# Performance work log

Hardware: AMD Instinct MI355X
Metric: run time of the kernel (lower is better)

## Reference

```python
import jax, jax.numpy as jnp
import numpy as np

EPS = 1e-8        # slot-attention epsilon
LN_EPS = 1e-5     # torch LayerNorm default
NUM_ITERS = 3

def _ln(x, g, b):
    m = jnp.mean(x, axis=-1, keepdims=True)
    v = jnp.var(x, axis=-1, keepdims=True)
    return (x - m) * jax.lax.rsqrt(v + LN_EPS) * g + b

def setup_inputs() -> dict:
    key = jax.random.key(0)
    ks = jax.random.split(key, 24)
    B, N, D, S, K, H = 64, 4096, 256, 256, 8, 512
    sc = 0.02
    return {
        "inputs": jax.random.normal(ks[0], (B, N, D), dtype=jnp.float32),
        "noise": jax.random.normal(ks[1], (B, K, S), dtype=jnp.float32),
        "slot_mu": jax.random.normal(ks[2], (1, 1, S)) * sc,
        "slot_log_sigma": jax.random.normal(ks[3], (1, 1, S)) * sc,
        "g_in": jnp.ones((D,)), "b_in": jnp.zeros((D,)),
        "g_sl": jnp.ones((S,)), "b_sl": jnp.zeros((S,)),
        "g_mlp": jnp.ones((S,)), "b_mlp": jnp.zeros((S,)),
        "Wq": jax.random.normal(ks[4], (S, S)) * sc,
        "Wk": jax.random.normal(ks[5], (S, D)) * sc,
        "Wv": jax.random.normal(ks[6], (S, D)) * sc,
        "W_ih": jax.random.normal(ks[7], (3 * S, S)) * sc,
        "W_hh": jax.random.normal(ks[8], (3 * S, S)) * sc,
        "b_ih": jnp.zeros((3 * S,)), "b_hh": jnp.zeros((3 * S,)),
        "W1": jax.random.normal(ks[9], (H, S)) * sc,
        "b1": jnp.zeros((H,)),
        "W2": jax.random.normal(ks[10], (S, H)) * sc,
        "b2": jnp.zeros((S,)),
    }

def _gru_cell(x, h, W_ih, W_hh, b_ih, b_hh):
    gi = x @ W_ih.T + b_ih
    gh = h @ W_hh.T + b_hh
    ir, iz, inn = jnp.split(gi, 3, axis=-1)
    hr, hz, hn = jnp.split(gh, 3, axis=-1)
    r = jax.nn.sigmoid(ir + hr)
    z = jax.nn.sigmoid(iz + hz)
    n = jnp.tanh(inn + r * hn)
    return (1.0 - z) * n + z * h

def reference(inputs, noise, slot_mu, slot_log_sigma, g_in, b_in, g_sl, b_sl,
              g_mlp, b_mlp, Wq, Wk, Wv, W_ih, W_hh, b_ih, b_hh, W1, b1, W2, b2):
    S = Wq.shape[0]
    slots = slot_mu + jnp.exp(slot_log_sigma) * noise          # [B,K,S]
    x = _ln(inputs, g_in, b_in)                                # [B,N,D]
    k = (x @ Wk.T) * (S ** -0.5)                               # [B,N,S]
    v = x @ Wv.T                                               # [B,N,S]
    for i in range(NUM_ITERS):
        slots_prev = slots
        q = _ln(slots, g_sl, b_sl) @ Wq.T                      # [B,K,S]
        attn_logits = jnp.einsum('bns,bks->bnk', k, q)         # [B,N,K]
        attn = jax.nn.softmax(attn_logits, axis=-1) + EPS      # softmax over slots
        attn = attn / jnp.sum(attn, axis=1, keepdims=True)     # normalize over inputs
        updates = jnp.einsum('bnk,bns->bks', attn, v)          # [B,K,S]
        slots = _gru_cell(updates, slots_prev, W_ih, W_hh, b_ih, b_hh)
        if i < NUM_ITERS - 1:
            h = jax.nn.relu(_ln(slots, g_mlp, b_mlp) @ W1.T + b1)
            slots = slots + (h @ W2.T + b2)
    return slots
```

## Files before the change

kernel.cpp:

```cpp
#include <hip/hip_runtime.h>
#include <math.h>

#define NB 64
#define NN 4096
#define ND 256
#define NS 256
#define NK 8
#define NH 512
#define NROW (NB*NN)
#define NSLOT (NB*NK)
#define EPSA 1e-8f
#define NCG 64

typedef unsigned short u16;
typedef unsigned int   u32;
typedef __bf16 bf16x8 __attribute__((ext_vector_type(8)));
typedef float  f32x4  __attribute__((ext_vector_type(4)));

__device__ __forceinline__ float bf2f(u16 u) {
  union { u32 i; float f; } v; v.i = ((u32)u) << 16; return v.f;
}
__device__ __forceinline__ u16 f2bf(float f) {
  union { float f; u32 i; } v; v.f = f;
  u32 x = v.i;
  return (u16)((x + 0x7FFFu + ((x >> 16) & 1u)) >> 16);
}
__device__ __forceinline__ u32 pack2(float a, float b) {
  return (u32)f2bf(a) | ((u32)f2bf(b) << 16);
}

#define OFF_XBF    0ULL
#define OFF_KG     134217728ULL
#define OFF_VTG    268435456ULL
#define OFF_SLOTS  402653184ULL
#define OFF_QBF    403177472ULL
#define OFF_UPDP   403439616ULL
#define OFF_SUMSP  436994048ULL
#define OFF_WC     437125120ULL
#define OFF_WQT    437387264ULL
#define OFF_WIHT   437649408ULL
#define OFF_WHHT   438435840ULL
#define OFF_W1T    439222272ULL
#define OFF_W2T    439746560ULL

__global__ __launch_bounds__(256) void prep_kernel(
    const float* __restrict__ Wq, const float* __restrict__ Wk, const float* __restrict__ Wv,
    const float* __restrict__ Wih, const float* __restrict__ Whh,
    const float* __restrict__ W1, const float* __restrict__ W2,
    u16* __restrict__ Wc, float* __restrict__ WqT, float* __restrict__ WihT,
    float* __restrict__ WhhT, float* __restrict__ W1T, float* __restrict__ W2T)
{
  int idx = blockIdx.x * 256 + threadIdx.x;
  if (idx < 512*256) {
    int j = idx >> 8, d = idx & 255;
    float w = (j < 256) ? Wk[idx] * 0.0625f : Wv[idx - 65536];
    Wc[idx] = f2bf(w);
    W1T[d*512 + j] = W1[idx];
  }
  if (idx < 256*256) {
    int j = idx >> 8, d = idx & 255;
    WqT[d*256 + j] = Wq[idx];
  }
  if (idx < 768*256) {
    int j = idx >> 8, d = idx & 255;
    WihT[d*768 + j] = Wih[idx];
    WhhT[d*768 + j] = Whh[idx];
  }
  if (idx < 256*512) {
    int j = idx >> 9, h = idx & 511;
    W2T[h*256 + j] = W2[idx];
  }
}

__global__ __launch_bounds__(256) void slots_init_kernel(
    const float* __restrict__ noise, const float* __restrict__ mu,
    const float* __restrict__ lsig, float* __restrict__ slots)
{
  int idx = blockIdx.x * 256 + threadIdx.x;
  int s = idx & 255;
  slots[idx] = mu[s] + expf(lsig[s]) * noise[idx];
}

__global__ __launch_bounds__(256) void ln_cast_kernel(
    const float* __restrict__ x, const float* __restrict__ g, const float* __restrict__ bb,
    u16* __restrict__ out)
{
  int row = blockIdx.x * 4 + (threadIdx.x >> 6);
  int lane = threadIdx.x & 63;
  float4 xv = *(const float4*)(x + (size_t)row * 256 + lane * 4);
  float s  = xv.x + xv.y + xv.z + xv.w;
  float sq = xv.x*xv.x + xv.y*xv.y + xv.z*xv.z + xv.w*xv.w;
  #pragma unroll
  for (int m = 32; m >= 1; m >>= 1) { s += __shfl_xor(s, m, 64); sq += __shfl_xor(sq, m, 64); }
  float mean = s * (1.f/256.f);
  float rstd = rsqrtf(sq * (1.f/256.f) - mean*mean + 1e-5f);
  float4 gv = *(const float4*)(g + lane*4);
  float4 bv = *(const float4*)(bb + lane*4);
  ushort4 o;
  o.x = f2bf((xv.x - mean) * rstd * gv.x + bv.x);
  o.y = f2bf((xv.y - mean) * rstd * gv.y + bv.y);
  o.z = f2bf((xv.z - mean) * rstd * gv.z + bv.z);
  o.w = f2bf((xv.w - mean) * rstd * gv.w + bv.w);
  *(ushort4*)(out + (size_t)row * 256 + lane*4) = o;
}

__global__ __launch_bounds__(256) void gemm_kv_kernel(
    const u16* __restrict__ A, const u16* __restrict__ Bt,
    u16* __restrict__ kg, u16* __restrict__ vtg)
{
  __shared__ u16 smem[17408];
  u16* As = smem;
  u16* Bs = smem + 4096;
  const int tid = threadIdx.x;
  const int lane = tid & 63;
  const int wv = tid >> 6;
  const int bm = blockIdx.x;
  const int bn = blockIdx.y;
  const int wm = (wv & 1) * 64;
  const int wn = (wv >> 1) * 64;

  f32x4 acc[4][4] = {};

  for (int k0 = 0; k0 < 256; k0 += 32) {
    #pragma unroll
    for (int r = 0; r < 2; ++r) {
      int off = ((r*4 + wv) << 10) + lane*16;
      int row = off >> 6;
      int col = (off & 63) >> 1;
      const u16* ga = A  + (size_t)(bm*128 + row) * 256 + k0 + col;
      const u16* gb = Bt + (size_t)(bn*128 + row) * 256 + k0 + col;
      __builtin_amdgcn_global_load_lds(
        (const __attribute__((address_space(1))) u32*)ga,
        (__attribute__((address_space(3))) u32*)((char*)As + off), 16, 0, 0);
      __builtin_amdgcn_global_load_lds(
        (const __attribute__((address_space(1))) u32*)gb,
        (__attribute__((address_space(3))) u32*)((char*)Bs + off), 16, 0, 0);
    }
    __syncthreads();
    bf16x8 af[4], bfr[4];
    #pragma unroll
    for (int t4 = 0; t4 < 4; ++t4) {
      af[t4]  = *(const bf16x8*)&As[(wm + t4*16 + (lane & 15)) * 32 + (lane >> 4) * 8];
      bfr[t4] = *(const bf16x8*)&Bs[(wn + t4*16 + (lane & 15)) * 32 + (lane >> 4) * 8];
    }
    #pragma unroll
    for (int mt = 0; mt < 4; ++mt)
      #pragma unroll
      for (int nt = 0; nt < 4; ++nt)
        acc[mt][nt] = __builtin_amdgcn_mfma_f32_16x16x32_bf16(af[mt], bfr[nt], acc[mt][nt], 0, 0, 0);
    __syncthreads();
  }
  const int cr = (lane >> 4) * 4;
  const int cc = lane & 15;
  if (bn < 2) {
    #pragma unroll
    for (int mt = 0; mt < 4; ++mt)
      #pragma unroll
      for (int nt = 0; nt < 4; ++nt)
        #pragma unroll
        for (int r = 0; r < 4; ++r) {
          size_t row = (size_t)(bm*128 + wm + mt*16 + cr + r);
          int col = bn*128 + wn + nt*16 + cc;
          kg[row * 256 + col] = f2bf(acc[mt][nt][r]);
        }
  } else {
    #pragma unroll
    for (int mt = 0; mt < 4; ++mt)
      #pragma unroll
      for (int nt = 0; nt < 4; ++nt) {
        int c  = wn + nt*16 + cc;
        int r0 = wm + mt*16 + cr;
        u32* p = (u32*)&smem[c*136 + r0];
        p[0] = pack2(acc[mt][nt][0], acc[mt][nt][1]);
        p[1] = pack2(acc[mt][nt][2], acc[mt][nt][3]);
      }
    __syncthreads();
    int c = tid >> 1, half = tid & 1;
    int d = (bn - 2) * 128 + c;
    const u16* srcp = &smem[c*136 + half*64];
    u16* dstp = vtg + (size_t)(bm >> 5)*1048576 + (size_t)d*4096 + (bm & 31)*128 + half*64;
    #pragma unroll
    for (int i = 0; i < 8; ++i)
      *(uint4*)(dstp + i*8) = *(const uint4*)(srcp + i*8);
  }
}

__global__ __launch_bounds__(256) void q_kernel(
    const float* __restrict__ slots, const float* __restrict__ gw, const float* __restrict__ bw,
    const float* __restrict__ WqT, u16* __restrict__ qbf)
{
  __shared__ float ln[2][256];
  int t = threadIdx.x, wv = t >> 6, lane = t & 63;
  int base = blockIdx.x * 2;
  if (wv < 2) {
    int row = base + wv;
    float4 xv = *(const float4*)(slots + (size_t)row*256 + lane*4);
    float s  = xv.x + xv.y + xv.z + xv.w;
    float sq = xv.x*xv.x + xv.y*xv.y + xv.z*xv.z + xv.w*xv.w;
    #pragma unroll
    for (int m = 32; m >= 1; m >>= 1) { s += __shfl_xor(s, m, 64); sq += __shfl_xor(sq, m, 64); }
    float mean = s * (1.f/256.f);
    float rstd = rsqrtf(sq * (1.f/256.f) - mean*mean + 1e-5f);
    float4 gv = *(const float4*)(gw + lane*4);
    float4 bv = *(const float4*)(bw + lane*4);
    ln[wv][lane*4+0] = (xv.x - mean)*rstd*gv.x + bv.x;
    ln[wv][lane*4+1] = (xv.y - mean)*rstd*gv.y + bv.y;
    ln[wv][lane*4+2] = (xv.z - mean)*rstd*gv.z + bv.z;
    ln[wv][lane*4+3] = (xv.w - mean)*rstd*gv.w + bv.w;
  }
  __syncthreads();
  float a0 = 0.f, a1 = 0.f;
  for (int d = 0; d < 256; ++d) {
    float w = WqT[d*256 + t];
    a0 += ln[0][d] * w;
    a1 += ln[1][d] * w;
  }
  qbf[(size_t)base*256 + t]     = f2bf(a0);
  qbf[(size_t)(base+1)*256 + t] = f2bf(a1);
}

__global__ __launch_bounds__(256) void attn_kernel(
    const u16* __restrict__ kg, const u16* __restrict__ vtg, const u16* __restrict__ qbf,
    float* __restrict__ updp, float* __restrict__ sums_p)
{
  __shared__ u16 tile[16384];
  __shared__ u16 attnT[16*72];
  __shared__ float sums_w[4][8];
  const int b = blockIdx.x, cg = blockIdx.y;
  const int t = threadIdx.x, w = t >> 6, lane = t & 63;
  const int L15 = lane & 15, q4 = lane >> 4;
  const int n0 = cg*64;
  const int slot = L15 & 7;

  bf16x8 vb[2][4];
  #pragma unroll
  for (int ks = 0; ks < 2; ++ks)
    #pragma unroll
    for (int dt = 0; dt < 4; ++dt) {
      int d = (dt*4 + w)*16 + L15;
      vb[ks][dt] = *(const bf16x8*)(vtg + (size_t)b*1048576 + (size_t)d*4096 + n0 + ks*32 + q4*8);
    }
  bf16x8 qf[8];
  {
    const u16* qp = qbf + ((size_t)b*8 + slot)*256;
    #pragma unroll
    for (int ks = 0; ks < 8; ++ks)
      qf[ks] = *(const bf16x8*)(qp + ks*32 + q4*8);
  }
  {
    const u16* srcbase = kg + (size_t)(b*4096 + n0)*256;
    #pragma unroll
    for (int j = 0; j < 8; ++j) {
      int i = w*8 + j;
      int n = i*2 + (lane >> 5);
      int p = lane & 31;
      int c = (p & 24) | ((p ^ n) & 7);
      const u16* src = srcbase + (size_t)n*256 + c*8;
      __builtin_amdgcn_global_load_lds(
        (const __attribute__((address_space(1))) u32*)src,
        (__attribute__((address_space(3))) u32*)((char*)tile + i*1024 + lane*16), 16, 0, 0);
    }
  }
  __syncthreads();

  f32x4 lg = {};
  {
    int n = w*16 + L15;
    #pragma unroll
    for (int ks = 0; ks < 8; ++ks) {
      int cck = ks*4 + q4;
      int p = (cck & 24) | ((cck ^ n) & 7);
      bf16x8 af = *(const bf16x8*)&tile[n*256 + p*8];
      lg = __builtin_amdgcn_mfma_f32_16x16x32_bf16(af, qf[ks], lg, 0, 0, 0);
    }
  }
  float av[4], tot = 0.f;
  #pragma unroll
  for (int r = 0; r < 4; ++r) {
    float val = lg[r];
    float mx = val;
    mx = fmaxf(mx, __shfl_xor(mx, 1, 64));
    mx = fmaxf(mx, __shfl_xor(mx, 2, 64));
    mx = fmaxf(mx, __shfl_xor(mx, 4, 64));
    float e = expf(val - mx);
    float se = e;
    se += __shfl_xor(se, 1, 64);
    se += __shfl_xor(se, 2, 64);
    se += __shfl_xor(se, 4, 64);
    av[r] = e / se + EPSA;
    tot += av[r];
  }
  if (L15 < 8) {
    u32* p = (u32*)&attnT[L15*72 + w*16 + q4*4];
    p[0] = pack2(av[0], av[1]);
    p[1] = pack2(av[2], av[3]);
  }
  tot += __shfl_xor(tot, 16, 64);
  tot += __shfl_xor(tot, 32, 64);
  if (q4 == 0 && L15 < 8) sums_w[w][L15] = tot;
  __syncthreads();

  f32x4 accp[4] = {};
  #pragma unroll
  for (int ks = 0; ks < 2; ++ks) {
    bf16x8 pa = *(const bf16x8*)&attnT[slot*72 + ks*32 + q4*8];
    #pragma unroll
    for (int dt = 0; dt < 4; ++dt)
      accp[dt] = __builtin_amdgcn_mfma_f32_16x16x32_bf16(pa, vb[ks][dt], accp[dt], 0, 0, 0);
  }
  if (q4 < 2) {
    float* up = updp + ((size_t)(b*NCG + cg))*2048;
    #pragma unroll
    for (int dt = 0; dt < 4; ++dt) {
      int d = (dt*4 + w)*16 + L15;
      #pragma unroll
      for (int r = 0; r < 4; ++r)
        up[(q4*4 + r)*256 + d] = accp[dt][r];
    }
  }
  if (t < 8)
    sums_p[(b*NCG + cg)*8 + t] = sums_w[0][t] + sums_w[1][t] + sums_w[2][t] + sums_w[3][t];
}

__global__ __launch_bounds__(256) void grumlp_kernel(
    const float* __restrict__ updp, const float* __restrict__ sums_p,
    const float* __restrict__ WihT, const float* __restrict__ WhhT,
    const float* __restrict__ bih, const float* __restrict__ bhh,
    const float* __restrict__ gm, const float* __restrict__ bm,
    const float* __restrict__ W1T, const float* __restrict__ b1,
    const float* __restrict__ W2T, const float* __restrict__ b2,
    float* __restrict__ slots, int do_mlp)
{
  __shared__ float xs[4][256], hs[4][256];
  __shared__ float ln[4][256];
  __shared__ float hb[4][512];
  int t = threadIdx.x, w = t >> 6, lane = t & 63;
  int base = blockIdx.x * 4;
  #pragma unroll
  for (int g = 0; g < 4; ++g) {
    int row = base + g;
    int b = row >> 3, s = row & 7;
    float u = 0.f, sm = 0.f;
    for (int c = 0; c < NCG; ++c) {
      u  += updp[((size_t)(b*NCG + c)*8 + s)*256 + t];
      sm += sums_p[(b*NCG + c)*8 + s];
    }
    xs[g][t] = u / sm;
    hs[g][t] = slots[(size_t)row*256 + t];
  }
  __syncthreads();
  float ra[4] = {}, za[4] = {}, ia[4] = {}, ha[4] = {};
  for (int d = 0; d < 256; ++d) {
    float wir = WihT[d*768 + t], wiz = WihT[d*768 + 256 + t], win = WihT[d*768 + 512 + t];
    float whr = WhhT[d*768 + t], whz = WhhT[d*768 + 256 + t], whn = WhhT[d*768 + 512 + t];
    #pragma unroll
    for (int g = 0; g < 4; ++g) {
      float xx = xs[g][d], hh = hs[g][d];
      ra[g] += xx*wir + hh*whr;
      za[g] += xx*wiz + hh*whz;
      ia[g] += xx*win;
      ha[g] += hh*whn;
    }
  }
  float bir = bih[t], biz = bih[256+t], bin = bih[512+t];
  float bhr = bhh[t], bhz = bhh[256+t], bhn = bhh[512+t];
  float nv[4];
  #pragma unroll
  for (int g = 0; g < 4; ++g) {
    float r  = 1.f/(1.f + expf(-(ra[g] + bir + bhr)));
    float z  = 1.f/(1.f + expf(-(za[g] + biz + bhz)));
    float nn = tanhf(ia[g] + bin + r*(ha[g] + bhn));
    nv[g] = (1.f - z)*nn + z*hs[g][t];
  }
  if (!do_mlp) {
    #pragma unroll
    for (int g = 0; g < 4; ++g)
      slots[(size_t)(base+g)*256 + t] = nv[g];
    return;
  }
  #pragma unroll
  for (int g = 0; g < 4; ++g) xs[g][t] = nv[g];
  __syncthreads();
  {
    float4 xv = *(const float4*)&xs[w][lane*4];
    float s  = xv.x + xv.y + xv.z + xv.w;
    float sq = xv.x*xv.x + xv.y*xv.y + xv.z*xv.z + xv.w*xv.w;
    #pragma unroll
    for (int m = 32; m >= 1; m >>= 1) { s += __shfl_xor(s, m, 64); sq += __shfl_xor(sq, m, 64); }
    float mean = s * (1.f/256.f);
    float rstd = rsqrtf(sq * (1.f/256.f) - mean*mean + 1e-5f);
    float4 gv = *(const float4*)(gm + lane*4);
    float4 bv = *(const float4*)(bm + lane*4);
    ln[w][lane*4+0] = (xv.x - mean)*rstd*gv.x + bv.x;
    ln[w][lane*4+1] = (xv.y - mean)*rstd*gv.y + bv.y;
    ln[w][lane*4+2] = (xv.z - mean)*rstd*gv.z + bv.z;
    ln[w][lane*4+3] = (xv.w - mean)*rstd*gv.w + bv.w;
  }
  __syncthreads();
  float h0[4] = {}, h1[4] = {};
  for (int d = 0; d < 256; ++d) {
    float w0 = W1T[d*512 + t], w1 = W1T[d*512 + 256 + t];
    #pragma unroll
    for (int g = 0; g < 4; ++g) { float l = ln[g][d]; h0[g] += l*w0; h1[g] += l*w1; }
  }
  float bb0 = b1[t], bb1 = b1[256 + t];
  #pragma unroll
  for (int g = 0; g < 4; ++g) {
    hb[g][t]       = fmaxf(h0[g] + bb0, 0.f);
    hb[g][256 + t] = fmaxf(h1[g] + bb1, 0.f);
  }
  __syncthreads();
  float o[4] = {};
  for (int hh = 0; hh < 512; ++hh) {
    float ww = W2T[hh*256 + t];
    #pragma unroll
    for (int g = 0; g < 4; ++g) o[g] += hb[g][hh] * ww;
  }
  float b2v = b2[t];
  #pragma unroll
  for (int g = 0; g < 4; ++g)
    slots[(size_t)(base+g)*256 + t] = xs[g][t] + o[g] + b2v;
}

extern "C" void kernel_launch(void* const* d_in, const int* in_sizes, int n_in,
                              void* d_out, int out_size, void* d_ws, size_t ws_size,
                              hipStream_t stream)
{
  (void)in_sizes; (void)n_in; (void)out_size; (void)ws_size;
  const float* inputs = (const float*)d_in[0];
  const float* noise  = (const float*)d_in[1];
  const float* mu     = (const float*)d_in[2];
  const float* lsig   = (const float*)d_in[3];
  const float* g_in   = (const float*)d_in[4];
  const float* b_in   = (const float*)d_in[5];
  const float* g_sl   = (const float*)d_in[6];
  const float* b_sl   = (const float*)d_in[7];
  const float* g_mlp  = (const float*)d_in[8];
  const float* b_mlp  = (const float*)d_in[9];
  const float* Wq     = (const float*)d_in[10];
  const float* Wk     = (const float*)d_in[11];
  const float* Wv     = (const float*)d_in[12];
  const float* Wih    = (const float*)d_in[13];
  const float* Whh    = (const float*)d_in[14];
  const float* bih    = (const float*)d_in[15];
  const float* bhh    = (const float*)d_in[16];
  const float* W1     = (const float*)d_in[17];
  const float* b1     = (const float*)d_in[18];
  const float* W2     = (const float*)d_in[19];
  const float* b2     = (const float*)d_in[20];

  char* ws = (char*)d_ws;
  u16*   x_bf   = (u16*)  (ws + OFF_XBF);
  u16*   kg     = (u16*)  (ws + OFF_KG);
  u16*   vtg    = (u16*)  (ws + OFF_VTG);
  float* slots  = (float*)(ws + OFF_SLOTS);
  u16*   qb     = (u16*)  (ws + OFF_QBF);
  float* updp   = (float*)(ws + OFF_UPDP);
  float* sums_p = (float*)(ws + OFF_SUMSP);
  u16*   Wc     = (u16*)  (ws + OFF_WC);
  float* WqT    = (float*)(ws + OFF_WQT);
  float* WihT   = (float*)(ws + OFF_WIHT);
  float* WhhT   = (float*)(ws + OFF_WHHT);
  float* W1T    = (float*)(ws + OFF_W1T);
  float* W2T    = (float*)(ws + OFF_W2T);

  prep_kernel<<<768, 256, 0, stream>>>(Wq, Wk, Wv, Wih, Whh, W1, W2,
                                       Wc, WqT, WihT, WhhT, W1T, W2T);
  slots_init_kernel<<<512, 256, 0, stream>>>(noise, mu, lsig, slots);
  ln_cast_kernel<<<NROW/4, 256, 0, stream>>>(inputs, g_in, b_in, x_bf);
  gemm_kv_kernel<<<dim3(NROW/128, 4), 256, 0, stream>>>(x_bf, Wc, kg, vtg);

  for (int it = 0; it < 3; ++it) {
    q_kernel<<<NSLOT/2, 256, 0, stream>>>(slots, g_sl, b_sl, WqT, qb);
    attn_kernel<<<dim3(NB, NCG), 256, 0, stream>>>(kg, vtg, qb, updp, sums_p);
    grumlp_kernel<<<NSLOT/4, 256, 0, stream>>>(updp, sums_p, WihT, WhhT, bih, bhh,
                                               g_mlp, b_mlp, W1T, b1, W2T, b2,
                                               slots, (it < 2) ? 1 : 0);
  }
  hipMemcpyAsync(d_out, slots, (size_t)NSLOT*NS*sizeof(float),
                 hipMemcpyDeviceToDevice, stream);
}
```

Before: 1.131 ms.

## Store K/V in MFMA-fragment layout, enlarge attention chunks, fuse q-projection into GRU kernel

The KV GEMM now writes K and V directly in a pre-tiled layout that matches the MFMA fragment order. Each attention block can then load operand fragments straight from global memory without staging through LDS. Attention blocks now cover 256 inputs instead of 64, which cuts the partial-sum count the GRU kernel must reduce, and the GEMM grid is flattened. The slot LayerNorm and Wq projection move into the tail of the GRU/MLP kernel, removing a launch per iteration. In exchange, the GRU kernel handles 2 slots per block, doubling its block count and weight re-reads, and the scattered 2-byte stores in the GEMM epilogue may be less efficient.

```diff
diff --git a/kernel.cpp b/kernel.cpp
--- a/kernel.cpp
+++ b/kernel.cpp
@@ -10,16 +10,13 @@
 #define NROW (NB*NN)
 #define NSLOT (NB*NK)
 #define EPSA 1e-8f
-#define NCG 64
+#define NCG 16
 
 typedef unsigned short u16;
 typedef unsigned int   u32;
 typedef __bf16 bf16x8 __attribute__((ext_vector_type(8)));
 typedef float  f32x4  __attribute__((ext_vector_type(4)));
 
-__device__ __forceinline__ float bf2f(u16 u) {
-  union { u32 i; float f; } v; v.i = ((u32)u) << 16; return v.f;
-}
 __device__ __forceinline__ u16 f2bf(float f) {
   union { float f; u32 i; } v; v.f = f;
   u32 x = v.i;
@@ -30,18 +27,18 @@
 }
 
 #define OFF_XBF    0ULL
-#define OFF_KG     134217728ULL
-#define OFF_VTG    268435456ULL
+#define OFF_KPRE   134217728ULL
+#define OFF_VPRE   268435456ULL
 #define OFF_SLOTS  402653184ULL
 #define OFF_QBF    403177472ULL
 #define OFF_UPDP   403439616ULL
-#define OFF_SUMSP  436994048ULL
-#define OFF_WC     437125120ULL
-#define OFF_WQT    437387264ULL
-#define OFF_WIHT   437649408ULL
-#define OFF_WHHT   438435840ULL
-#define OFF_W1T    439222272ULL
-#define OFF_W2T    439746560ULL
+#define OFF_SUMSP  411828224ULL
+#define OFF_WC     411860992ULL
+#define OFF_WQT    412123136ULL
+#define OFF_WIHT   412385280ULL
+#define OFF_WHHT   413171712ULL
+#define OFF_W1T    413958144ULL
+#define OFF_W2T    414482432ULL
 
 __global__ __launch_bounds__(256) void prep_kernel(
     const float* __restrict__ Wq, const float* __restrict__ Wk, const float* __restrict__ Wv,
@@ -106,16 +103,15 @@
 
 __global__ __launch_bounds__(256) void gemm_kv_kernel(
     const u16* __restrict__ A, const u16* __restrict__ Bt,
-    u16* __restrict__ kg, u16* __restrict__ vtg)
-{
-  __shared__ u16 smem[17408];
-  u16* As = smem;
-  u16* Bs = smem + 4096;
+    u16* __restrict__ kpre, u16* __restrict__ vpre)
+{
+  __shared__ u16 As[4096];
+  __shared__ u16 Bs[4096];
   const int tid = threadIdx.x;
   const int lane = tid & 63;
   const int wv = tid >> 6;
-  const int bm = blockIdx.x;
-  const int bn = blockIdx.y;
+  const int bm = blockIdx.x >> 2;
+  const int bn = blockIdx.x & 3;
   const int wm = (wv & 1) * 64;
   const int wn = (wv >> 1) * 64;
 
@@ -154,34 +150,34 @@
   const int cc = lane & 15;
   if (bn < 2) {
     #pragma unroll
-    for (int mt = 0; mt < 4; ++mt)
+    for (int mt = 0; mt < 4; ++mt) {
+      int ntile = bm*8 + (wm >> 4) + mt;
       #pragma unroll
-      for (int nt = 0; nt < 4; ++nt)
+      for (int nt = 0; nt < 4; ++nt) {
+        int d = bn*128 + wn + nt*16 + cc;
+        size_t base = ((size_t)ntile*8 + (d >> 5))*512 + ((d >> 3) & 3)*8 + (d & 7);
+        #pragma unroll
+        for (int r = 0; r < 4; ++r)
+          kpre[base + (cr + r)*32] = f2bf(acc[mt][nt][r]);
+      }
+    }
+  } else {
+    #pragma unroll
+    for (int mt = 0; mt < 4; ++mt) {
+      #pragma unroll
+      for (int nt = 0; nt < 4; ++nt) {
+        int dv = (bn - 2)*128 + wn + nt*16 + cc;
         #pragma unroll
         for (int r = 0; r < 4; ++r) {
-          size_t row = (size_t)(bm*128 + wm + mt*16 + cr + r);
-          int col = bn*128 + wn + nt*16 + cc;
-          kg[row * 256 + col] = f2bf(acc[mt][nt][r]);
+          int n = bm*128 + wm + mt*16 + cr + r;
+          int b = n >> 12, nn = n & 4095;
+          size_t addr = (size_t)b*1048576
+                      + ((size_t)(dv >> 4)*128 + (nn >> 5))*512
+                      + (dv & 15)*32 + ((nn >> 3) & 3)*8 + (nn & 7);
+          vpre[addr] = f2bf(acc[mt][nt][r]);
         }
-  } else {
-    #pragma unroll
-    for (int mt = 0; mt < 4; ++mt)
-      #pragma unroll
-      for (int nt = 0; nt < 4; ++nt) {
-        int c  = wn + nt*16 + cc;
-        int r0 = wm + mt*16 + cr;
-        u32* p = (u32*)&smem[c*136 + r0];
-        p[0] = pack2(acc[mt][nt][0], acc[mt][nt][1]);
-        p[1] = pack2(acc[mt][nt][2], acc[mt][nt][3]);
       }
-    __syncthreads();
-    int c = tid >> 1, half = tid & 1;
-    int d = (bn - 2) * 128 + c;
-    const u16* srcp = &smem[c*136 + half*64];
-    u16* dstp = vtg + (size_t)(bm >> 5)*1048576 + (size_t)d*4096 + (bm & 31)*128 + half*64;
-    #pragma unroll
-    for (int i = 0; i < 8; ++i)
-      *(uint4*)(dstp + i*8) = *(const uint4*)(srcp + i*8);
+    }
   }
 }
 
@@ -220,26 +216,16 @@
 }
 
 __global__ __launch_bounds__(256) void attn_kernel(
-    const u16* __restrict__ kg, const u16* __restrict__ vtg, const u16* __restrict__ qbf,
+    const u16* __restrict__ kpre, const u16* __restrict__ vpre, const u16* __restrict__ qbf,
     float* __restrict__ updp, float* __restrict__ sums_p)
 {
-  __shared__ u16 tile[16384];
-  __shared__ u16 attnT[16*72];
+  __shared__ u16 attnT[8*264];
   __shared__ float sums_w[4][8];
   const int b = blockIdx.x, cg = blockIdx.y;
   const int t = threadIdx.x, w = t >> 6, lane = t & 63;
   const int L15 = lane & 15, q4 = lane >> 4;
-  const int n0 = cg*64;
   const int slot = L15 & 7;
 
-  bf16x8 vb[2][4];
-  #pragma unroll
-  for (int ks = 0; ks < 2; ++ks)
-    #pragma unroll
-    for (int dt = 0; dt < 4; ++dt) {
-      int d = (dt*4 + w)*16 + L15;
-      vb[ks][dt] = *(const bf16x8*)(vtg + (size_t)b*1048576 + (size_t)d*4096 + n0 + ks*32 + q4*8);
-    }
   bf16x8 qf[8];
   {
     const u16* qp = qbf + ((size_t)b*8 + slot)*256;
@@ -247,53 +233,39 @@
     for (int ks = 0; ks < 8; ++ks)
       qf[ks] = *(const bf16x8*)(qp + ks*32 + q4*8);
   }
-  {
-    const u16* srcbase = kg + (size_t)(b*4096 + n0)*256;
-    #pragma unroll
-    for (int j = 0; j < 8; ++j) {
-      int i = w*8 + j;
-      int n = i*2 + (lane >> 5);
-      int p = lane & 31;
-      int c = (p & 24) | ((p ^ n) & 7);
-      const u16* src = srcbase + (size_t)n*256 + c*8;
-      __builtin_amdgcn_global_load_lds(
-        (const __attribute__((address_space(1))) u32*)src,
-        (__attribute__((address_space(3))) u32*)((char*)tile + i*1024 + lane*16), 16, 0, 0);
-    }
-  }
-  __syncthreads();
-
-  f32x4 lg = {};
-  {
-    int n = w*16 + L15;
+
+  const u16* kbase = kpre + (size_t)(b*256 + cg*16)*8*512 + L15*32 + q4*8;
+  float tot = 0.f;
+  #pragma unroll
+  for (int i = 0; i < 4; ++i) {
+    f32x4 lg = {};
+    const u16* ktile = kbase + (size_t)(w*4 + i)*8*512;
     #pragma unroll
     for (int ks = 0; ks < 8; ++ks) {
-      int cck = ks*4 + q4;
-      int p = (cck & 24) | ((cck ^ n) & 7);
-      bf16x8 af = *(const bf16x8*)&tile[n*256 + p*8];
+      bf16x8 af = *(const bf16x8*)(ktile + ks*512);
       lg = __builtin_amdgcn_mfma_f32_16x16x32_bf16(af, qf[ks], lg, 0, 0, 0);
     }
-  }
-  float av[4], tot = 0.f;
-  #pragma unroll
-  for (int r = 0; r < 4; ++r) {
-    float val = lg[r];
-    float mx = val;
-    mx = fmaxf(mx, __shfl_xor(mx, 1, 64));
-    mx = fmaxf(mx, __shfl_xor(mx, 2, 64));
-    mx = fmaxf(mx, __shfl_xor(mx, 4, 64));
-    float e = expf(val - mx);
-    float se = e;
-    se += __shfl_xor(se, 1, 64);
-    se += __shfl_xor(se, 2, 64);
-    se += __shfl_xor(se, 4, 64);
-    av[r] = e / se + EPSA;
-    tot += av[r];
-  }
-  if (L15 < 8) {
-    u32* p = (u32*)&attnT[L15*72 + w*16 + q4*4];
-    p[0] = pack2(av[0], av[1]);
-    p[1] = pack2(av[2], av[3]);
+    float av[4];
+    #pragma unroll
+    for (int r = 0; r < 4; ++r) {
+      float val = lg[r];
+      float mx = val;
+      mx = fmaxf(mx, __shfl_xor(mx, 1, 64));
+      mx = fmaxf(mx, __shfl_xor(mx, 2, 64));
+      mx = fmaxf(mx, __shfl_xor(mx, 4, 64));
+      float e = expf(val - mx);
+      float se = e;
+      se += __shfl_xor(se, 1, 64);
+      se += __shfl_xor(se, 2, 64);
+      se += __shfl_xor(se, 4, 64);
+      av[r] = e / se + EPSA;
+      tot += av[r];
+    }
+    if (L15 < 8) {
+      u32* p = (u32*)&attnT[slot*264 + (w*4 + i)*16 + q4*4];
+      p[0] = pack2(av[0], av[1]);
+      p[1] = pack2(av[2], av[3]);
+    }
   }
   tot += __shfl_xor(tot, 16, 64);
   tot += __shfl_xor(tot, 32, 64);
@@ -301,18 +273,22 @@
   __syncthreads();
 
   f32x4 accp[4] = {};
-  #pragma unroll
-  for (int ks = 0; ks < 2; ++ks) {
-    bf16x8 pa = *(const bf16x8*)&attnT[slot*72 + ks*32 + q4*8];
-    #pragma unroll
-    for (int dt = 0; dt < 4; ++dt)
-      accp[dt] = __builtin_amdgcn_mfma_f32_16x16x32_bf16(pa, vb[ks][dt], accp[dt], 0, 0, 0);
+  const u16* vbase = vpre + (size_t)b*1048576 + L15*32 + q4*8;
+  #pragma unroll
+  for (int ks2 = 0; ks2 < 8; ++ks2) {
+    bf16x8 pa = *(const bf16x8*)&attnT[slot*264 + ks2*32 + q4*8];
+    #pragma unroll
+    for (int dt = 0; dt < 4; ++dt) {
+      int dtile = w*4 + dt;
+      bf16x8 vb = *(const bf16x8*)(vbase + (size_t)(dtile*128 + cg*8 + ks2)*512);
+      accp[dt] = __builtin_amdgcn_mfma_f32_16x16x32_bf16(pa, vb, accp[dt], 0, 0, 0);
+    }
   }
   if (q4 < 2) {
     float* up = updp + ((size_t)(b*NCG + cg))*2048;
     #pragma unroll
     for (int dt = 0; dt < 4; ++dt) {
-      int d = (dt*4 + w)*16 + L15;
+      int d = (w*4 + dt)*16 + L15;
       #pragma unroll
       for (int r = 0; r < 4; ++r)
         up[(q4*4 + r)*256 + d] = accp[dt][r];
@@ -329,18 +305,21 @@
     const float* __restrict__ gm, const float* __restrict__ bm,
     const float* __restrict__ W1T, const float* __restrict__ b1,
     const float* __restrict__ W2T, const float* __restrict__ b2,
-    float* __restrict__ slots, int do_mlp)
-{
-  __shared__ float xs[4][256], hs[4][256];
-  __shared__ float ln[4][256];
-  __shared__ float hb[4][512];
+    const float* __restrict__ gq, const float* __restrict__ bq,
+    const float* __restrict__ WqT,
+    float* __restrict__ slots, u16* __restrict__ qbf, int do_mlp)
+{
+  __shared__ float xs[2][256], hs[2][256];
+  __shared__ float ln[2][256];
+  __shared__ float hb[2][512];
   int t = threadIdx.x, w = t >> 6, lane = t & 63;
-  int base = blockIdx.x * 4;
-  #pragma unroll
-  for (int g = 0; g < 4; ++g) {
+  int base = blockIdx.x * 2;
+  #pragma unroll
+  for (int g = 0; g < 2; ++g) {
     int row = base + g;
     int b = row >> 3, s = row & 7;
     float u = 0.f, sm = 0.f;
+    #pragma unroll
     for (int c = 0; c < NCG; ++c) {
       u  += updp[((size_t)(b*NCG + c)*8 + s)*256 + t];
       sm += sums_p[(b*NCG + c)*8 + s];
@@ -349,12 +328,12 @@
     hs[g][t] = slots[(size_t)row*256 + t];
   }
   __syncthreads();
-  float ra[4] = {}, za[4] = {}, ia[4] = {}, ha[4] = {};
+  float ra[2] = {}, za[2] = {}, ia[2] = {}, ha[2] = {};
   for (int d = 0; d < 256; ++d) {
     float wir = WihT[d*768 + t], wiz = WihT[d*768 + 256 + t], win = WihT[d*768 + 512 + t];
     float whr = WhhT[d*768 + t], whz = WhhT[d*768 + 256 + t], whn = WhhT[d*768 + 512 + t];
     #pragma unroll
-    for (int g = 0; g < 4; ++g) {
+    for (int g = 0; g < 2; ++g) {
       float xx = xs[g][d], hh = hs[g][d];
       ra[g] += xx*wir + hh*whr;
       za[g] += xx*wiz + hh*whz;
@@ -364,9 +343,9 @@
   }
   float bir = bih[t], biz = bih[256+t], bin = bih[512+t];
   float bhr = bhh[t], bhz = bhh[256+t], bhn = bhh[512+t];
-  float nv[4];
-  #pragma unroll
-  for (int g = 0; g < 4; ++g) {
+  float nv[2];
+  #pragma unroll
+  for (int g = 0; g < 2; ++g) {
     float r  = 1.f/(1.f + expf(-(ra[g] + bir + bhr)));
     float z  = 1.f/(1.f + expf(-(za[g] + biz + bhz)));
     float nn = tanhf(ia[g] + bin + r*(ha[g] + bhn));
@@ -374,14 +353,14 @@
   }
   if (!do_mlp) {
     #pragma unroll
-    for (int g = 0; g < 4; ++g)
+    for (int g = 0; g < 2; ++g)
       slots[(size_t)(base+g)*256 + t] = nv[g];
     return;
   }
   #pragma unroll
-  for (int g = 0; g < 4; ++g) xs[g][t] = nv[g];
-  __syncthreads();
-  {
+  for (int g = 0; g < 2; ++g) xs[g][t] = nv[g];
+  __syncthreads();
+  if (w < 2) {
     float4 xv = *(const float4*)&xs[w][lane*4];
     float s  = xv.x + xv.y + xv.z + xv.w;
     float sq = xv.x*xv.x + xv.y*xv.y + xv.z*xv.z + xv.w*xv.w;
@@ -397,29 +376,57 @@
     ln[w][lane*4+3] = (xv.w - mean)*rstd*gv.w + bv.w;
   }
   __syncthreads();
-  float h0[4] = {}, h1[4] = {};
+  float h0[2] = {}, h1[2] = {};
   for (int d = 0; d < 256; ++d) {
     float w0 = W1T[d*512 + t], w1 = W1T[d*512 + 256 + t];
     #pragma unroll
-    for (int g = 0; g < 4; ++g) { float l = ln[g][d]; h0[g] += l*w0; h1[g] += l*w1; }
+    for (int g = 0; g < 2; ++g) { float l = ln[g][d]; h0[g] += l*w0; h1[g] += l*w1; }
   }
   float bb0 = b1[t], bb1 = b1[256 + t];
   #pragma unroll
-  for (int g = 0; g < 4; ++g) {
+  for (int g = 0; g < 2; ++g) {
     hb[g][t]       = fmaxf(h0[g] + bb0, 0.f);
     hb[g][256 + t] = fmaxf(h1[g] + bb1, 0.f);
   }
   __syncthreads();
-  float o[4] = {};
+  float o[2] = {};
   for (int hh = 0; hh < 512; ++hh) {
     float ww = W2T[hh*256 + t];
     #pragma unroll
-    for (int g = 0; g < 4; ++g) o[g] += hb[g][hh] * ww;
+    for (int g = 0; g < 2; ++g) o[g] += hb[g][hh] * ww;
   }
   float b2v = b2[t];
   #pragma unroll
-  for (int g = 0; g < 4; ++g)
-    slots[(size_t)(base+g)*256 + t] = xs[g][t] + o[g] + b2v;
+  for (int g = 0; g < 2; ++g) {
+    float snew = xs[g][t] + o[g] + b2v;
+    slots[(size_t)(base+g)*256 + t] = snew;
+    xs[g][t] = snew;
+  }
+  __syncthreads();
+  if (w < 2) {
+    float4 xv = *(const float4*)&xs[w][lane*4];
+    float s  = xv.x + xv.y + xv.z + xv.w;
+    float sq = xv.x*xv.x + xv.y*xv.y + xv.z*xv.z + xv.w*xv.w;
+    #pragma unroll
+    for (int m = 32; m >= 1; m >>= 1) { s += __shfl_xor(s, m, 64); sq += __shfl_xor(sq, m, 64); }
+    float mean = s * (1.f/256.f);
+    float rstd = rsqrtf(sq * (1.f/256.f) - mean*mean + 1e-5f);
+    float4 gv = *(const float4*)(gq + lane*4);
+    float4 bv = *(const float4*)(bq + lane*4);
+    ln[w][lane*4+0] = (xv.x - mean)*rstd*gv.x + bv.x;
+    ln[w][lane*4+1] = (xv.y - mean)*rstd*gv.y + bv.y;
+    ln[w][lane*4+2] = (xv.z - mean)*rstd*gv.z + bv.z;
+    ln[w][lane*4+3] = (xv.w - mean)*rstd*gv.w + bv.w;
+  }
+  __syncthreads();
+  float a0 = 0.f, a1 = 0.f;
+  for (int d = 0; d < 256; ++d) {
+    float wq = WqT[d*256 + t];
+    a0 += ln[0][d] * wq;
+    a1 += ln[1][d] * wq;
+  }
+  qbf[(size_t)base*256 + t]     = f2bf(a0);
+  qbf[(size_t)(base+1)*256 + t] = f2bf(a1);
 }
 
 extern "C" void kernel_launch(void* const* d_in, const int* in_sizes, int n_in,
@@ -451,8 +458,8 @@
 
   char* ws = (char*)d_ws;
   u16*   x_bf   = (u16*)  (ws + OFF_XBF);
-  u16*   kg     = (u16*)  (ws + OFF_KG);
-  u16*   vtg    = (u16*)  (ws + OFF_VTG);
+  u16*   kpre   = (u16*)  (ws + OFF_KPRE);
+  u16*   vpre   = (u16*)  (ws + OFF_VPRE);
   float* slots  = (float*)(ws + OFF_SLOTS);
   u16*   qb     = (u16*)  (ws + OFF_QBF);
   float* updp   = (float*)(ws + OFF_UPDP);
@@ -468,14 +475,15 @@
                                        Wc, WqT, WihT, WhhT, W1T, W2T);
   slots_init_kernel<<<512, 256, 0, stream>>>(noise, mu, lsig, slots);
   ln_cast_kernel<<<NROW/4, 256, 0, stream>>>(inputs, g_in, b_in, x_bf);
-  gemm_kv_kernel<<<dim3(NROW/128, 4), 256, 0, stream>>>(x_bf, Wc, kg, vtg);
+  gemm_kv_kernel<<<8192, 256, 0, stream>>>(x_bf, Wc, kpre, vpre);
+  q_kernel<<<NSLOT/2, 256, 0, stream>>>(slots, g_sl, b_sl, WqT, qb);
 
   for (int it = 0; it < 3; ++it) {
-    q_kernel<<<NSLOT/2, 256, 0, stream>>>(slots, g_sl, b_sl, WqT, qb);
-    attn_kernel<<<dim3(NB, NCG), 256, 0, stream>>>(kg, vtg, qb, updp, sums_p);
-    grumlp_kernel<<<NSLOT/4, 256, 0, stream>>>(updp, sums_p, WihT, WhhT, bih, bhh,
+    attn_kernel<<<dim3(NB, NCG), 256, 0, stream>>>(kpre, vpre, qb, updp, sums_p);
+    grumlp_kernel<<<NSLOT/2, 256, 0, stream>>>(updp, sums_p, WihT, WhhT, bih, bhh,
                                                g_mlp, b_mlp, W1T, b1, W2T, b2,
-                                               slots, (it < 2) ? 1 : 0);
+                                               g_sl, b_sl, WqT,
+                                               slots, qb, (it < 2) ? 1 : 0);
   }
   hipMemcpyAsync(d_out, slots, (size_t)NSLOT*NS*sizeof(float),
                  hipMemcpyDeviceToDevice, stream);
```

Measured after the change: 1.017 ms. 10.1% less time.
